# Kernel optimization log

Measured on AMD Instinct MI355X. Metric: run time of the kernel, lower is better.

Reference implementation:

```python
import jax, jax.numpy as jnp
import numpy as np

E, V, F, D = 500000, 50000, 100000, 128

def setup_inputs() -> dict:
    key = jax.random.key(0)
    ks = jax.random.split(key, 8)
    return {
        "prev_m_f_to_v": jax.random.normal(ks[0], (E, D), jnp.float32),
        "variable": jax.random.normal(ks[1], (V, D), jnp.float32),
        "factor": jax.random.normal(ks[2], (F, D), jnp.float32),
        "edge_attr": jax.random.normal(ks[3], (E, D), jnp.float32),
        "v_to_f": jax.random.randint(ks[4], (E,), 0, V, jnp.int32),
        "f_to_v": jax.random.randint(ks[5], (E,), 0, F, jnp.int32),
        "Wv": jax.random.normal(ks[6], (3 * D, D), jnp.float32) * (1.0 / np.sqrt(3 * D)),
        "bv": jnp.zeros((D,), jnp.float32),
        "Wf": jax.random.normal(ks[7], (3 * D, D), jnp.float32) * (1.0 / np.sqrt(3 * D)),
        "bf": jnp.zeros((D,), jnp.float32),
    }

def _mlp(x, y, edge_attr, W, b):
    # update(): concat along features then Linear(3d->d) + relu
    h = jnp.concatenate((x, y, edge_attr), axis=-1)  # [E, 3D]
    return jax.nn.relu(h @ W + b)                    # [E, D]

def reference(prev_m_f_to_v, variable, factor, edge_attr, v_to_f, f_to_v, Wv, bv, Wf, bf):
    nV = variable.shape[0]
    nF = factor.shape[0]
    # scatter-sum of factor->variable messages onto variables
    sum_f_to_v = jax.ops.segment_sum(prev_m_f_to_v, v_to_f, num_segments=nV)  # [V, D]
    # BP exclusion: gather back and subtract own message
    m_v_to_f = sum_f_to_v[v_to_f] - prev_m_f_to_v                             # [E, D]
    m_v_to_f = _mlp(variable[v_to_f], m_v_to_f, edge_attr, Wv, bv)            # [E, D]
    # scatter-sum of variable->factor messages onto factors
    sum_v_to_f = jax.ops.segment_sum(m_v_to_f, f_to_v, num_segments=nF)       # [F, D]
    m_f_to_v = sum_v_to_f[f_to_v] - m_v_to_f                                  # [E, D]
    m_f_to_v = _mlp(factor[f_to_v], m_f_to_v, edge_attr, Wf, bf)              # [E, D]
    new_factor = sum_v_to_f + factor
    new_variable = sum_f_to_v + variable
    return (m_f_to_v, new_factor, new_variable)
```

## Files before the change

### kernel.cpp

```cpp
#include <hip/hip_runtime.h>

typedef __attribute__((ext_vector_type(8))) __bf16 bf16x8;
typedef __attribute__((ext_vector_type(2))) __bf16 bf16x2;
typedef __attribute__((ext_vector_type(4))) float f32x4;

__device__ inline bf16x8 pack8(f32x4 u0, f32x4 u1) {
    bf16x8 r;
    r[0] = (__bf16)u0[0]; r[1] = (__bf16)u0[1]; r[2] = (__bf16)u0[2]; r[3] = (__bf16)u0[3];
    r[4] = (__bf16)u1[0]; r[5] = (__bf16)u1[1]; r[6] = (__bf16)u1[2]; r[7] = (__bf16)u1[3];
    return r;
}

__global__ void pack_w(const float* __restrict__ W, __bf16* __restrict__ out,
                       int baseA, float sA, int baseB, float sB) {
    int i = blockIdx.x * blockDim.x + threadIdx.x;
    if (i >= 256 * 128) return;
    int k = i >> 7, d = i & 127;
    float v = (k < 128) ? sA * W[(long)(baseA + k) * 128 + d]
                        : sB * W[(long)(baseB + (k - 128)) * 128 + d];
    int t = k >> 5, n = d >> 4;
    int lane = (d & 15) | (((k >> 3) & 3) << 4);
    int j = k & 7;
    out[((long)(t * 8 + n) * 64 + lane) * 8 + j] = (__bf16)v;
}


__global__ void hist_kernel(const int* __restrict__ v_to_f, const int* __restrict__ f_to_v,
                            int* __restrict__ counts, int V, int E) {
    int stride = gridDim.x * blockDim.x;
    for (int e = blockIdx.x * blockDim.x + threadIdx.x; e < E; e += stride) {
        atomicAdd(&counts[v_to_f[e]], 1);
        atomicAdd(&counts[V + f_to_v[e]], 1);
    }
}

#define SCAN_BLOCK 256
#define SCAN_ELEMS 4

__global__ void scan_pass1(const int* __restrict__ counts, int* __restrict__ partials, int N) {
    int t = threadIdx.x;
    int base = blockIdx.x * (SCAN_BLOCK * SCAN_ELEMS) + t * SCAN_ELEMS;
    int s = 0;
#pragma unroll
    for (int j = 0; j < SCAN_ELEMS; ++j) {
        int i = base + j;
        if (i < N) s += counts[i];
    }
#pragma unroll
    for (int off = 1; off < 64; off <<= 1) s += __shfl_xor(s, off);
    __shared__ int lds[4];
    if ((t & 63) == 0) lds[t >> 6] = s;
    __syncthreads();
    if (t == 0) partials[blockIdx.x] = lds[0] + lds[1] + lds[2] + lds[3];
}

__global__ void scan_pass2(int* __restrict__ partials, int nb, int* __restrict__ offsets,
                           int N, int total) {
    int t = threadIdx.x;
    int v = (t < nb) ? partials[t] : 0;
    int lane = t & 63, w = t >> 6;
    int x = v;
#pragma unroll
    for (int off = 1; off < 64; off <<= 1) { int y = __shfl_up(x, off); if (lane >= off) x += y; }
    __shared__ int lds[4];
    if (lane == 63) lds[w] = x;
    __syncthreads();
    int add = 0;
    for (int i = 0; i < w; ++i) add += lds[i];
    if (t < nb) partials[t] = x + add - v;
    if (t == 0) offsets[N] = total;
}

__global__ void scan_pass3(const int* __restrict__ counts, const int* __restrict__ partials,
                           int* __restrict__ offsets, int* __restrict__ cursors, int N) {
    int t = threadIdx.x;
    int base = blockIdx.x * (SCAN_BLOCK * SCAN_ELEMS) + t * SCAN_ELEMS;
    int c[SCAN_ELEMS];
    int s = 0;
#pragma unroll
    for (int j = 0; j < SCAN_ELEMS; ++j) {
        int i = base + j;
        c[j] = (i < N) ? counts[i] : 0;
        s += c[j];
    }
    int lane = t & 63, w = t >> 6;
    int x = s;
#pragma unroll
    for (int off = 1; off < 64; off <<= 1) { int y = __shfl_up(x, off); if (lane >= off) x += y; }
    __shared__ int lds[4];
    if (lane == 63) lds[w] = x;
    __syncthreads();
    int add = 0;
    for (int i = 0; i < w; ++i) add += lds[i];
    int run = x + add - s + partials[blockIdx.x];
#pragma unroll
    for (int j = 0; j < SCAN_ELEMS; ++j) {
        int i = base + j;
        if (i < N) { offsets[i] = run; cursors[i] = run; }
        run += c[j];
    }
}

__global__ void fill_kernel(const int* __restrict__ v_to_f, const int* __restrict__ f_to_v,
                            int* __restrict__ cursors, int* __restrict__ bucket, int V, int E) {
    int stride = gridDim.x * blockDim.x;
    for (int e = blockIdx.x * blockDim.x + threadIdx.x; e < E; e += stride) {
        int p = atomicAdd(&cursors[v_to_f[e]], 1);
        bucket[p] = e;
        int q = atomicAdd(&cursors[V + f_to_v[e]], 1);
        bucket[q] = e;
    }
}


__global__ __launch_bounds__(256) void gsum_f32(
    const float* __restrict__ src, const int* __restrict__ bucket,
    const int* __restrict__ offsets, int toff,
    const float* __restrict__ addtab, float* __restrict__ sumout,
    float* __restrict__ addout, int T) {
    int gw = (int)((blockIdx.x * (long)blockDim.x + threadIdx.x) >> 6);
    if (gw >= T) return;
    int lane = threadIdx.x & 63;
    int start = offsets[toff + gw], end = offsets[toff + gw + 1];
    float ax = 0.f, ay = 0.f, bx = 0.f, by = 0.f;
    int i = start;
    for (; i + 1 < end; i += 2) {
        int e0 = bucket[i], e1 = bucket[i + 1];
        float2 v0 = *(const float2*)(src + (long)e0 * 128 + lane * 2);
        float2 v1 = *(const float2*)(src + (long)e1 * 128 + lane * 2);
        ax += v0.x; ay += v0.y; bx += v1.x; by += v1.y;
    }
    if (i < end) {
        int e0 = bucket[i];
        float2 v0 = *(const float2*)(src + (long)e0 * 128 + lane * 2);
        ax += v0.x; ay += v0.y;
    }
    ax += bx; ay += by;
    long o = (long)gw * 128 + lane * 2;
    *(float2*)(sumout + o) = make_float2(ax, ay);
    float2 a = *(const float2*)(addtab + o);
    *(float2*)(addout + o) = make_float2(ax + a.x, ay + a.y);
}

__global__ __launch_bounds__(256) void gsum_bf16(
    const __bf16* __restrict__ src, const int* __restrict__ bucket,
    const int* __restrict__ offsets, int toff,
    const float* __restrict__ addtab, float* __restrict__ sumout,
    float* __restrict__ addout, int T) {
    int gw = (int)((blockIdx.x * (long)blockDim.x + threadIdx.x) >> 6);
    if (gw >= T) return;
    int lane = threadIdx.x & 63;
    int start = offsets[toff + gw], end = offsets[toff + gw + 1];
    float ax = 0.f, ay = 0.f, bx = 0.f, by = 0.f;
    int i = start;
    for (; i + 1 < end; i += 2) {
        int e0 = bucket[i], e1 = bucket[i + 1];
        bf16x2 v0 = *(const bf16x2*)(src + (long)e0 * 128 + lane * 2);
        bf16x2 v1 = *(const bf16x2*)(src + (long)e1 * 128 + lane * 2);
        ax += (float)v0[0]; ay += (float)v0[1];
        bx += (float)v1[0]; by += (float)v1[1];
    }
    if (i < end) {
        int e0 = bucket[i];
        bf16x2 v0 = *(const bf16x2*)(src + (long)e0 * 128 + lane * 2);
        ax += (float)v0[0]; ay += (float)v0[1];
    }
    ax += bx; ay += by;
    long o = (long)gw * 128 + lane * 2;
    *(float2*)(sumout + o) = make_float2(ax, ay);
    float2 a = *(const float2*)(addtab + o);
    *(float2*)(addout + o) = make_float2(ax + a.x, ay + a.y);
}

__global__ __launch_bounds__(256, 4) void table_gemm(
    const float* __restrict__ src0, const float* __restrict__ src1,
    const __bf16* __restrict__ WT, const float* __restrict__ bias,
    __bf16* __restrict__ out, int T) {
    const int wave = threadIdx.x >> 6;
    const int lane = threadIdx.x & 63;
    const int row = lane & 15;
    const int kch = lane >> 4;
    const long wbase = ((long)blockIdx.x * 4 + wave) * 32;

    const float* p0[2]; const float* p1[2];
#pragma unroll
    for (int rb = 0; rb < 2; ++rb) {
        long r = wbase + rb * 16 + row;
        long rl = (r < T) ? r : (T - 1);
        p0[rb] = src0 + rl * 128 + kch * 8;
        p1[rb] = src1 + rl * 128 + kch * 8;
    }

    f32x4 acc[8][2];
#pragma unroll
    for (int n = 0; n < 8; ++n) {
        acc[n][0] = (f32x4){0.f, 0.f, 0.f, 0.f};
        acc[n][1] = (f32x4){0.f, 0.f, 0.f, 0.f};
    }

#pragma unroll
    for (int t = 0; t < 8; ++t) {
        bf16x8 a[2];
#pragma unroll
        for (int rb = 0; rb < 2; ++rb) {
            const float* p = (t < 4) ? (p0[rb] + t * 32) : (p1[rb] + (t - 4) * 32);
            f32x4 u0 = *(const f32x4*)p;
            f32x4 u1 = *(const f32x4*)(p + 4);
            a[rb] = pack8(u0, u1);
        }
        const __bf16* bbase = WT + (long)t * 8 * 512 + lane * 8;
#pragma unroll
        for (int n = 0; n < 8; ++n) {
            bf16x8 b = *(const bf16x8*)(bbase + n * 512);
            acc[n][0] = __builtin_amdgcn_mfma_f32_16x16x32_bf16(a[0], b, acc[n][0], 0, 0, 0);
            acc[n][1] = __builtin_amdgcn_mfma_f32_16x16x32_bf16(a[1], b, acc[n][1], 0, 0, 0);
        }
    }

    const int colbase = lane & 15;
    const int orow = (lane >> 4) * 4;
#pragma unroll
    for (int n = 0; n < 8; ++n) {
        int col = n * 16 + colbase;
        float bz = bias[col];
#pragma unroll
        for (int rb = 0; rb < 2; ++rb)
#pragma unroll
            for (int rr = 0; rr < 4; ++rr) {
                long r = wbase + rb * 16 + orow + rr;
                if (r < T) out[r * 128 + col] = (__bf16)(acc[n][rb][rr] + bz);
            }
    }
}

template <int PHASE>
__global__ __launch_bounds__(256, 4) void edge_gemm(
    const float* __restrict__ prevf, const __bf16* __restrict__ prevb,
    const float* __restrict__ eattr, const __bf16* __restrict__ WT,
    const __bf16* __restrict__ G, const int* __restrict__ idx,
    __bf16* __restrict__ outb, float* __restrict__ outf, int E) {
    const int wave = threadIdx.x >> 6;
    const int lane = threadIdx.x & 63;
    const int row = lane & 15;
    const int kch = lane >> 4;
    const long wbase = ((long)blockIdx.x * 4 + wave) * 32;

    const float* e0[2]; const float* pf[2]; const __bf16* pb[2];
#pragma unroll
    for (int rb = 0; rb < 2; ++rb) {
        long e = wbase + rb * 16 + row;
        long el = (e < E) ? e : (E - 1);
        e0[rb] = eattr + el * 128 + kch * 8;
        if (PHASE == 1) pf[rb] = prevf + el * 128 + kch * 8;
        else            pb[rb] = prevb + el * 128 + kch * 8;
    }

    const int orow = (lane >> 4) * 4;
    int gidx[2][4];
#pragma unroll
    for (int rb = 0; rb < 2; ++rb)
#pragma unroll
        for (int rr = 0; rr < 4; ++rr) {
            long eo = wbase + rb * 16 + orow + rr;
            gidx[rb][rr] = idx[(eo < E) ? eo : (E - 1)];
        }

    f32x4 acc[8][2];
#pragma unroll
    for (int n = 0; n < 8; ++n) {
        acc[n][0] = (f32x4){0.f, 0.f, 0.f, 0.f};
        acc[n][1] = (f32x4){0.f, 0.f, 0.f, 0.f};
    }

#pragma unroll
    for (int t = 0; t < 8; ++t) {
        bf16x8 a[2];
#pragma unroll
        for (int rb = 0; rb < 2; ++rb) {
            if (t < 4) {
                if (PHASE == 1) {
                    f32x4 u0 = *(const f32x4*)(pf[rb] + t * 32);
                    f32x4 u1 = *(const f32x4*)(pf[rb] + t * 32 + 4);
                    a[rb] = pack8(u0, u1);
                } else {
                    a[rb] = *(const bf16x8*)(pb[rb] + t * 32);
                }
            } else {
                f32x4 u0 = *(const f32x4*)(e0[rb] + (t - 4) * 32);
                f32x4 u1 = *(const f32x4*)(e0[rb] + (t - 4) * 32 + 4);
                a[rb] = pack8(u0, u1);
            }
        }
        const __bf16* bbase = WT + (long)t * 8 * 512 + lane * 8;
#pragma unroll
        for (int n = 0; n < 8; ++n) {
            bf16x8 b = *(const bf16x8*)(bbase + n * 512);
            acc[n][0] = __builtin_amdgcn_mfma_f32_16x16x32_bf16(a[0], b, acc[n][0], 0, 0, 0);
            acc[n][1] = __builtin_amdgcn_mfma_f32_16x16x32_bf16(a[1], b, acc[n][1], 0, 0, 0);
        }
    }

    const int colbase = lane & 15;
#pragma unroll
    for (int n = 0; n < 8; ++n) {
        int col = n * 16 + colbase;
#pragma unroll
        for (int rb = 0; rb < 2; ++rb)
#pragma unroll
            for (int rr = 0; rr < 4; ++rr) {
                long eo = wbase + rb * 16 + orow + rr;
                if (eo < E) {
                    float v = acc[n][rb][rr] + (float)G[(long)gidx[rb][rr] * 128 + col];
                    v = v > 0.f ? v : 0.f;
                    if (PHASE == 1) outb[eo * 128 + col] = (__bf16)v;
                    else            outf[eo * 128 + col] = v;
                }
            }
    }
}

extern "C" void kernel_launch(void* const* d_in, const int* in_sizes, int n_in,
                              void* d_out, int out_size, void* d_ws, size_t ws_size,
                              hipStream_t stream) {
    const float* prev_m   = (const float*)d_in[0];
    const float* variable = (const float*)d_in[1];
    const float* factor   = (const float*)d_in[2];
    const float* eattr    = (const float*)d_in[3];
    const int*   v_to_f   = (const int*)d_in[4];
    const int*   f_to_v   = (const int*)d_in[5];
    const float* Wv       = (const float*)d_in[6];
    const float* bv       = (const float*)d_in[7];
    const float* Wf       = (const float*)d_in[8];
    const float* bf       = (const float*)d_in[9];

    const int E = in_sizes[0] / 128;
    const int V = in_sizes[1] / 128;
    const int F = in_sizes[2] / 128;
    const int NT = V + F;

    float* out_m        = (float*)d_out;
    float* out_factor   = out_m + (long)E * 128;
    float* out_variable = out_factor + (long)F * 128;

    char* ws = (char*)d_ws;
    float* sum_f_to_v = (float*)ws;  ws += (long)V * 128 * 4;
    float* sum_v_to_f = (float*)ws;  ws += (long)F * 128 * 4;
    __bf16* m1        = (__bf16*)ws; ws += (long)E * 128 * 2;
    __bf16* G1        = (__bf16*)ws; ws += (long)V * 128 * 2;
    __bf16* G2        = (__bf16*)ws; ws += (long)F * 128 * 2;
    __bf16* Wtab_v    = (__bf16*)ws; ws += 256 * 128 * 2;
    __bf16* Wedge_v   = (__bf16*)ws; ws += 256 * 128 * 2;
    __bf16* Wtab_f    = (__bf16*)ws; ws += 256 * 128 * 2;
    __bf16* Wedge_f   = (__bf16*)ws; ws += 256 * 128 * 2;
    int* counts       = (int*)ws;    ws += (long)NT * 4;
    int* offsets      = (int*)ws;    ws += (long)(NT + 1) * 4;
    int* cursors      = (int*)ws;    ws += (long)NT * 4;
    int* bucket       = (int*)ws;    ws += (long)2 * E * 4;
    int* partials     = (int*)ws;    ws += 256 * 4;

    hipMemsetAsync(counts, 0, (size_t)NT * 4, stream);

    pack_w<<<dim3(128), dim3(256), 0, stream>>>(Wv, Wtab_v,  0,   1.f, 128, 1.f);
    pack_w<<<dim3(128), dim3(256), 0, stream>>>(Wv, Wedge_v, 128, -1.f, 256, 1.f);
    pack_w<<<dim3(128), dim3(256), 0, stream>>>(Wf, Wtab_f,  0,   1.f, 128, 1.f);
    pack_w<<<dim3(128), dim3(256), 0, stream>>>(Wf, Wedge_f, 128, -1.f, 256, 1.f);

    hist_kernel<<<dim3(2048), dim3(256), 0, stream>>>(v_to_f, f_to_v, counts, V, E);
    int nb = (NT + SCAN_BLOCK * SCAN_ELEMS - 1) / (SCAN_BLOCK * SCAN_ELEMS);
    scan_pass1<<<dim3(nb), dim3(SCAN_BLOCK), 0, stream>>>(counts, partials, NT);
    scan_pass2<<<dim3(1), dim3(SCAN_BLOCK), 0, stream>>>(partials, nb, offsets, NT, 2 * E);
    scan_pass3<<<dim3(nb), dim3(SCAN_BLOCK), 0, stream>>>(counts, partials, offsets, cursors, NT);
    fill_kernel<<<dim3(2048), dim3(256), 0, stream>>>(v_to_f, f_to_v, cursors, bucket, V, E);

    gsum_f32<<<dim3((V + 3) / 4), dim3(256), 0, stream>>>(
        prev_m, bucket, offsets, 0, variable, sum_f_to_v, out_variable, V);

    table_gemm<<<dim3((V + 127) / 128), dim3(256), 0, stream>>>(
        variable, sum_f_to_v, Wtab_v, bv, G1, V);

    int eblocks = (E + 127) / 128;
    edge_gemm<1><<<dim3(eblocks), dim3(256), 0, stream>>>(
        prev_m, nullptr, eattr, Wedge_v, G1, v_to_f, m1, nullptr, E);

    gsum_bf16<<<dim3((F + 3) / 4), dim3(256), 0, stream>>>(
        m1, bucket, offsets, V, factor, sum_v_to_f, out_factor, F);

    table_gemm<<<dim3((F + 127) / 128), dim3(256), 0, stream>>>(
        factor, sum_v_to_f, Wtab_f, bf, G2, F);

    edge_gemm<2><<<dim3(eblocks), dim3(256), 0, stream>>>(
        nullptr, m1, eattr, Wedge_f, G2, f_to_v, nullptr, out_m, E);
}
```

Measured before the change: 864.1 us.

## Stage edge GEMM A-operand through triple-buffered LDS via global_load_lds

Replaces direct per-lane global loads of the A operand (prev messages and edge attributes) in edge_gemm with asynchronous global-to-LDS copies into a 3-deep ring, prefetching the next K-tile while the current one feeds the MFMAs. The LDS layout uses an XOR swizzle to avoid bank conflicts and gives each block 128 rows with coalesced 16-byte loads. The change adds 48KB of LDS per block and a barrier per K step, and lowers the launch-bounds occupancy hint from 4 to 3 blocks. Correctness relies on the barrier ordering of the async LDS loads.

```diff
diff --git a/kernel.cpp b/kernel.cpp
--- a/kernel.cpp
+++ b/kernel.cpp
@@ -3,6 +3,12 @@
 typedef __attribute__((ext_vector_type(8))) __bf16 bf16x8;
 typedef __attribute__((ext_vector_type(2))) __bf16 bf16x2;
 typedef __attribute__((ext_vector_type(4))) float f32x4;
+
+__device__ __forceinline__ void gload_lds16(const void* g, void* l) {
+    __builtin_amdgcn_global_load_lds(
+        (const __attribute__((address_space(1))) void*)g,
+        (__attribute__((address_space(3))) void*)l, 16, 0, 0);
+}
 
 __device__ inline bf16x8 pack8(f32x4 u0, f32x4 u1) {
     bf16x8 r;
@@ -234,34 +240,52 @@
 }
 
 template <int PHASE>
-__global__ __launch_bounds__(256, 4) void edge_gemm(
+__global__ __launch_bounds__(256, 3) void edge_gemm(
     const float* __restrict__ prevf, const __bf16* __restrict__ prevb,
     const float* __restrict__ eattr, const __bf16* __restrict__ WT,
     const __bf16* __restrict__ G, const int* __restrict__ idx,
     __bf16* __restrict__ outb, float* __restrict__ outf, int E) {
+    __shared__ char lds[3][16384];
     const int wave = threadIdx.x >> 6;
     const int lane = threadIdx.x & 63;
-    const int row = lane & 15;
+    const int row16 = lane & 15;
     const int kch = lane >> 4;
-    const long wbase = ((long)blockIdx.x * 4 + wave) * 32;
-
-    const float* e0[2]; const float* pf[2]; const __bf16* pb[2];
-#pragma unroll
-    for (int rb = 0; rb < 2; ++rb) {
-        long e = wbase + rb * 16 + row;
-        long el = (e < E) ? e : (E - 1);
-        e0[rb] = eattr + el * 128 + kch * 8;
-        if (PHASE == 1) pf[rb] = prevf + el * 128 + kch * 8;
-        else            pb[rb] = prevb + el * 128 + kch * 8;
-    }
-
-    const int orow = (lane >> 4) * 4;
+    const long brow = (long)blockIdx.x * 128;
+
+    auto stage = [&](int buf, int t) {
+        char* dst = &lds[buf][0];
+        if (PHASE == 2 && t < 4) {
+#pragma unroll
+            for (int q = 0; q < 2; ++q) {
+                int s0 = q * 256 + wave * 64;
+                int row = (s0 >> 2) + (lane >> 2);
+                int c = lane & 3;
+                int c2 = c ^ ((row >> 1) & 3);
+                long rowg = brow + row; if (rowg >= E) rowg = E - 1;
+                gload_lds16(prevb + rowg * 128 + t * 32 + c2 * 8, dst + s0 * 16);
+            }
+        } else {
+            const float* srcb = (PHASE == 1 && t < 4) ? (prevf + t * 32)
+                                                      : (eattr + (t - 4) * 32);
+#pragma unroll
+            for (int q = 0; q < 4; ++q) {
+                int s0 = q * 256 + wave * 64;
+                int row = (s0 >> 3) + (lane >> 3);
+                int c = lane & 7;
+                int c2 = c ^ (row & 7);
+                long rowg = brow + row; if (rowg >= E) rowg = E - 1;
+                gload_lds16(srcb + rowg * 128 + c2 * 4, dst + s0 * 16);
+            }
+        }
+    };
+
+    const int orow = kch * 4;
     int gidx[2][4];
 #pragma unroll
     for (int rb = 0; rb < 2; ++rb)
 #pragma unroll
         for (int rr = 0; rr < 4; ++rr) {
-            long eo = wbase + rb * 16 + orow + rr;
+            long eo = brow + wave * 32 + rb * 16 + orow + rr;
             gidx[rb][rr] = idx[(eo < E) ? eo : (E - 1)];
         }
 
@@ -272,22 +296,25 @@
         acc[n][1] = (f32x4){0.f, 0.f, 0.f, 0.f};
     }
 
+    stage(0, 0);
 #pragma unroll
     for (int t = 0; t < 8; ++t) {
+        __syncthreads();
+        if (t < 7) stage((t + 1) % 3, t + 1);
+        const char* cur = &lds[t % 3][0];
         bf16x8 a[2];
 #pragma unroll
         for (int rb = 0; rb < 2; ++rb) {
-            if (t < 4) {
-                if (PHASE == 1) {
-                    f32x4 u0 = *(const f32x4*)(pf[rb] + t * 32);
-                    f32x4 u1 = *(const f32x4*)(pf[rb] + t * 32 + 4);
-                    a[rb] = pack8(u0, u1);
-                } else {
-                    a[rb] = *(const bf16x8*)(pb[rb] + t * 32);
-                }
+            int row = wave * 32 + rb * 16 + row16;
+            if (PHASE == 2 && t < 4) {
+                int off = row * 64 + ((kch ^ ((row >> 1) & 3)) * 16);
+                a[rb] = *(const bf16x8*)(cur + off);
             } else {
-                f32x4 u0 = *(const f32x4*)(e0[rb] + (t - 4) * 32);
-                f32x4 u1 = *(const f32x4*)(e0[rb] + (t - 4) * 32 + 4);
+                int base = row * 128;
+                int s0 = (((kch * 2 + 0) ^ (row & 7)) * 16);
+                int s1 = (((kch * 2 + 1) ^ (row & 7)) * 16);
+                f32x4 u0 = *(const f32x4*)(cur + base + s0);
+                f32x4 u1 = *(const f32x4*)(cur + base + s1);
                 a[rb] = pack8(u0, u1);
             }
         }
@@ -308,7 +335,7 @@
         for (int rb = 0; rb < 2; ++rb)
 #pragma unroll
             for (int rr = 0; rr < 4; ++rr) {
-                long eo = wbase + rb * 16 + orow + rr;
+                long eo = brow + wave * 32 + rb * 16 + orow + rr;
                 if (eo < E) {
                     float v = acc[n][rb][rr] + (float)G[(long)gidx[rb][rr] * 128 + col];
                     v = v > 0.f ? v : 0.f;
```

After: 861.0 us. Within noise of the previous version (-0.4%).
